# Performance work log

Measured on AMD Instinct MI355X. Metric: run time of the kernel, lower is better.

The kernel has to match this reference:

```python
import jax, jax.numpy as jnp
import numpy as np

NEG_INF = -1000000000.0

N, T, D, H = 2, 4096, 512, 8
S = D // H  # size_per_head = 64


def setup_inputs() -> dict:
    key = jax.random.key(0)
    ks = jax.random.split(key, 6)
    scale = 1.0 / np.sqrt(D)
    return {
        "query": jax.random.normal(ks[0], (N, T, D), dtype=jnp.float32),
        "reference": jax.random.normal(ks[1], (N, T, D), dtype=jnp.float32),
        "padding_mask": jnp.zeros((N, 1, 1, T), dtype=jnp.float32),
        "Wq": jax.random.normal(ks[2], (D, H, S), dtype=jnp.float32) * scale,
        "Wk": jax.random.normal(ks[3], (D, H, S), dtype=jnp.float32) * scale,
        "Wv": jax.random.normal(ks[4], (D, H, S), dtype=jnp.float32) * scale,
        "Wo": jax.random.normal(ks[5], (H, S, D), dtype=jnp.float32) * scale,
    }


def reference(query, reference, padding_mask, Wq, Wk, Wv, Wo):
    # split projections: [N,T,D] x [D,H,S] -> [N,T,H,S]
    q = jnp.einsum("NTD,DHS->NTHS", query, Wq) * (S ** -0.5)
    k = jnp.einsum("NTD,DHS->NTHS", reference, Wk)
    v = jnp.einsum("NTD,DHS->NTHS", reference, Wv)
    # scores [N,H,Q,R]; mask is 0/1, scaled by NEG_INF (as in source)
    scores = jnp.einsum("NQHS,NRHS->NHQR", q, k) + padding_mask * NEG_INF
    probs = jax.nn.softmax(scores, axis=3)
    # dropout is identity (training=False)
    ctx = jnp.einsum("NHQR,NRHS->NQHS", probs, v)
    # merge projection: [N,Q,H,S] x [H,S,D] -> [N,Q,D]
    return jnp.einsum("NTHS,HSD->NTD", ctx, Wo)
```

## Files before the change

### kernel.cpp

```cpp
#include <hip/hip_runtime.h>
#include <stdint.h>

using u16    = unsigned short;
using u32    = unsigned int;
using short8 = __attribute__((ext_vector_type(8))) short;
using s16x4  = __attribute__((ext_vector_type(4))) short;
using f32x4  = __attribute__((ext_vector_type(4))) float;
using f32x16 = __attribute__((ext_vector_type(16))) float;
using i32x4  = __attribute__((ext_vector_type(4))) int;

constexpr float LOG2E = 1.44269504088896340736f;


__device__ __forceinline__ u16 f2bf(float f) {
  uint32_t u = __builtin_bit_cast(uint32_t, f);
  return (u16)((u + 0x7fffu + ((u >> 16) & 1u)) >> 16);
}

__device__ __forceinline__ void gload16(const void* g, void* l) {
  __builtin_amdgcn_global_load_lds(
      (const __attribute__((address_space(1))) unsigned int*)g,
      (__attribute__((address_space(3))) unsigned int*)l, 16, 0, 0);
}

__device__ __forceinline__ u32 cvtpk_bf16(float lo, float hi) {
  u32 r;
  asm("v_cvt_pk_bf16_f32 %0, %1, %2" : "=v"(r) : "v"(lo), "v"(hi));
  return r;
}

__device__ __forceinline__ f32x16 zero16() {
  f32x16 z;
#pragma unroll
  for (int i = 0; i < 16; ++i) z[i] = 0.f;
  return z;
}

__device__ __forceinline__ short8 ldfrag(const u16* s, int row, int kbyte) {
  int phys = (row << 7) + (kbyte ^ ((row & 7) << 4));
  return *(const short8*)((const char*)s + phys);
}

__global__ __launch_bounds__(256) void prep_kernel(
    const float4* __restrict__ qin, const float4* __restrict__ rin,
    const float* __restrict__ mask,
    const float* __restrict__ wq, const float* __restrict__ wk,
    const float* __restrict__ wv, const float* __restrict__ wo,
    u16* __restrict__ xq, u16* __restrict__ xr,
    u16* __restrict__ wqt, u16* __restrict__ wkt,
    u16* __restrict__ wvt, u16* __restrict__ wot,
    u16* __restrict__ kfr, int* __restrict__ mflag) {
  const int gid = blockIdx.x * blockDim.x + threadIdx.x;
  const int stride = gridDim.x * blockDim.x;
  for (int i = gid; i < (2 * 4096 * 512) / 4; i += stride) {
    float4 a = qin[i], b = rin[i];
    s16x4 va = {(short)f2bf(a.x), (short)f2bf(a.y), (short)f2bf(a.z), (short)f2bf(a.w)};
    s16x4 vb = {(short)f2bf(b.x), (short)f2bf(b.y), (short)f2bf(b.z), (short)f2bf(b.w)};
    *(s16x4*)(xq + i * 4) = va;
    *(s16x4*)(xr + i * 4) = vb;
  }
  for (int i = gid; i < 512 * 512; i += stride) {
    int orow = i >> 9, ocol = i & 511;
    int si = ocol * 512 + orow;
    wqt[i] = f2bf(wq[si]);
    wkt[i] = f2bf(wk[si]);
    wvt[i] = f2bf(wv[si]);
    wot[i] = f2bf(wo[si]);
  }
  for (int i = gid; i < 16 * 4096; i += stride) {
    int head = i >> 12, key = i & 4095;
    int nn = head >> 3;
    float mv = mask[nn * 4096 + key];
    float mt = mv * (-1.0e9f * LOG2E);
    int tile = key >> 5, lqk = key & 31;
    u16* base = kfr + (((size_t)(head * 128 + tile)) * 5 + 4) * 512;
    u16* p0 = base + (size_t)lqk * 8;
    u16* p1 = base + (size_t)(32 + lqk) * 8;
    p0[0] = f2bf(mt);
#pragma unroll
    for (int j = 1; j < 8; ++j) p0[j] = 0;
#pragma unroll
    for (int j = 0; j < 8; ++j) p1[j] = 0;
    unsigned long long any = __ballot(mv != 0.0f);
    if ((threadIdx.x & 63) == 0 && any != 0ULL) atomicOr(mflag, 1);
  }
}

__device__ __forceinline__ void gemm_core(const u16* __restrict__ A, const u16* __restrict__ Bt,
                                          int K, u16* As, u16* Bs, int tm0, int tn0,
                                          f32x4 acc[4][4]) {
  const int tid = threadIdx.x;
  const int wv = tid >> 6, ln = tid & 63;
  const int lr = ln & 15, hi = ln >> 4;
  const int wr = wv >> 1, wc = wv & 1;
  const size_t rowbytes = (size_t)K * 2;
  for (int k0 = 0; k0 < K; k0 += 64) {
    __syncthreads();
    const char* Ab = (const char*)A + (size_t)tm0 * rowbytes + (size_t)k0 * 2;
    const char* Bb = (const char*)Bt + (size_t)tn0 * rowbytes + (size_t)k0 * 2;
#pragma unroll
    for (int c = 0; c < 4; ++c) {
      int lin = wv * 4096 + c * 1024 + ln * 16;
      int row = lin >> 7;
      int cb = (lin & 127) ^ ((row & 7) << 4);
      gload16(Ab + (size_t)row * rowbytes + cb, (char*)As + wv * 4096 + c * 1024);
      gload16(Bb + (size_t)row * rowbytes + cb, (char*)Bs + wv * 4096 + c * 1024);
    }
    __syncthreads();
#pragma unroll
    for (int ks = 0; ks < 2; ++ks) {
      short8 af[4], bf[4];
#pragma unroll
      for (int m = 0; m < 4; ++m) af[m] = ldfrag(As, wr * 64 + m * 16 + lr, ks * 64 + hi * 16);
#pragma unroll
      for (int n = 0; n < 4; ++n) bf[n] = ldfrag(Bs, wc * 64 + n * 16 + lr, ks * 64 + hi * 16);
#pragma unroll
      for (int m = 0; m < 4; ++m)
#pragma unroll
        for (int n = 0; n < 4; ++n)
          acc[m][n] = __builtin_amdgcn_mfma_f32_16x16x32_bf16(af[m], bf[n], acc[m][n], 0, 0, 0);
    }
  }
}

__global__ __launch_bounds__(256) void qkv_gemm(
    const u16* __restrict__ xq, const u16* __restrict__ xr,
    const u16* __restrict__ wqt, const u16* __restrict__ wkt, const u16* __restrict__ wvt,
    u16* __restrict__ qo, u16* __restrict__ kfr, u16* __restrict__ vfr) {
  __shared__ u16 As[128 * 64];
  __shared__ u16 Bs[128 * 64];
  const int z = blockIdx.z;
  const u16* A  = (z == 0) ? xq : xr;
  const u16* Bt = (z == 0) ? wqt : (z == 1) ? wkt : wvt;
  const int tm0 = blockIdx.x * 128, tn0 = blockIdx.y * 128;
  f32x4 acc[4][4];
#pragma unroll
  for (int m = 0; m < 4; ++m)
#pragma unroll
    for (int n = 0; n < 4; ++n) { f32x4 zz = {0.f, 0.f, 0.f, 0.f}; acc[m][n] = zz; }
  gemm_core(A, Bt, 512, As, Bs, tm0, tn0, acc);

  const int tid = threadIdx.x, wv = tid >> 6, ln = tid & 63, lr = ln & 15, hi = ln >> 4;
  const int wr = wv >> 1, wc = wv & 1;
  const float scale = (z == 0) ? 0.125f * LOG2E : 1.0f;
#pragma unroll
  for (int m = 0; m < 4; ++m) {
#pragma unroll
    for (int n = 0; n < 4; ++n) {
#pragma unroll
      for (int r = 0; r < 4; ++r) {
        int rg = tm0 + wr * 64 + m * 16 + hi * 4 + r;
        int cg = tn0 + wc * 64 + n * 16 + lr;
        int nb = rg >> 12, t = rg & 4095;
        int h = cg >> 6, s = cg & 63;
        int head = nb * 8 + h;
        u16 b = f2bf(acc[m][n][r] * scale);
        if (z == 0) {
          qo[((size_t)head * 4096 + t) * 64 + s] = b;
        } else if (z == 1) {
          int tile = t >> 5, lqk = t & 31;
          int ks = s >> 4, hh = (s >> 3) & 1, j = s & 7;
          kfr[((((size_t)(head * 128 + tile)) * 5 + ks) * 64 + hh * 32 + lqk) * 8 + j] = b;
        } else {
          int tile = t >> 5, key5 = t & 31;
          int c = key5 >> 4, w = key5 & 15;
          int hh2 = (w >> 2) & 1;
          int j2 = (w & 3) + ((w >> 3) << 2);
          int st = s >> 5, lqs = s & 31;
          vfr[((((size_t)(head * 128 + tile)) * 4 + c * 2 + st) * 64 + hh2 * 32 + lqs) * 8 + j2] = b;
        }
      }
    }
  }
}

__global__ __launch_bounds__(512, 2) void attn15_kernel(
    const u16* __restrict__ q, const char* __restrict__ kfr, const char* __restrict__ vfr,
    u16* __restrict__ ctx, const int* __restrict__ mflag) {
  __shared__ __align__(16) char smem[4 * 32 * 65 * 4];
  __shared__ float cl[4][64];
  float (*cmbraw)[32][64] = (float(*)[32][64])smem;
  float (*cmb2)[32][65]   = (float(*)[32][65])smem;
  const int id = blockIdx.x;
  const int xcd = id & 7, slot = id >> 3;
  const int head = xcd * 2 + (slot >> 4);
  const int qb = slot & 15;
  const int n = head >> 3, h = head & 7;
  const int tid = threadIdx.x, wv = tid >> 6, ln = tid & 63;
  const int lq = ln & 31, hi = ln >> 5, hi4 = hi * 4;
  const int qt = wv & 3, kg = wv >> 2;
  const int q0 = qb * 256 + qt * 64;
  const bool aug = (*mflag != 0);

  short8 qfa[5], qfb[5];
  {
    const char* qp = (const char*)(q + (size_t)head * 4096 * 64) + (size_t)(q0 + lq) * 128 + hi * 16;
#pragma unroll
    for (int ks = 0; ks < 4; ++ks) {
      qfa[ks] = *(const short8*)(qp + ks * 32);
      qfb[ks] = *(const short8*)(qp + 32 * 128 + ks * 32);
    }
    short8 z = {0, 0, 0, 0, 0, 0, 0, 0};
    if (hi == 0) z[0] = (short)0x3F80;
    qfa[4] = z;
    qfb[4] = z;
  }

  const char* kp = kfr + (size_t)head * 655360 + (size_t)(kg * 64) * 5120 + ln * 16;
  const char* vp = vfr + (size_t)head * 524288 + (size_t)(kg * 64) * 4096 + ln * 16;

  short8 kA[5];
#pragma unroll
  for (int s = 0; s < 4; ++s) kA[s] = *(const short8*)(kp + s * 1024);
  if (aug) kA[4] = *(const short8*)(kp + 4 * 1024);
  kp += 5120;

  f32x16 cacc0a = zero16(), cacc1a = zero16();
  f32x16 cacc0b = zero16(), cacc1b = zero16();
  f32x16 la = zero16(), lb = zero16();

  for (int it = 0; it < 64; ++it) {
    short8 vt[4];
#pragma unroll
    for (int s = 0; s < 4; ++s) vt[s] = *(const short8*)(vp + s * 1024);
    vp += 4096;

    f32x16 Sa = zero16(), Sb = zero16();
    __builtin_amdgcn_s_setprio(1);
#pragma unroll
    for (int ks = 0; ks < 4; ++ks) {
      Sa = __builtin_amdgcn_mfma_f32_32x32x16_bf16(kA[ks], qfa[ks], Sa, 0, 0, 0);
      Sb = __builtin_amdgcn_mfma_f32_32x32x16_bf16(kA[ks], qfb[ks], Sb, 0, 0, 0);
    }
    if (aug) {
      Sa = __builtin_amdgcn_mfma_f32_32x32x16_bf16(kA[4], qfa[4], Sa, 0, 0, 0);
      Sb = __builtin_amdgcn_mfma_f32_32x32x16_bf16(kA[4], qfb[4], Sb, 0, 0, 0);
    }
    __builtin_amdgcn_s_setprio(0);

    short8 kN[5];
#pragma unroll
    for (int s = 0; s < 4; ++s) kN[s] = *(const short8*)(kp + s * 1024);
    if (aug) kN[4] = *(const short8*)(kp + 4 * 1024);
    kp += 5120;

    float pa_[16], pb_[16];
#pragma unroll
    for (int r = 0; r < 16; ++r) { pa_[r] = __builtin_amdgcn_exp2f(Sa[r]); la[r] += pa_[r]; }
#pragma unroll
    for (int r = 0; r < 16; ++r) { pb_[r] = __builtin_amdgcn_exp2f(Sb[r]); lb[r] += pb_[r]; }

    short8 pA0, pA1, pB0, pB1;
    {
      i32x4 f0 = {(int)cvtpk_bf16(pa_[0], pa_[1]), (int)cvtpk_bf16(pa_[2], pa_[3]),
                  (int)cvtpk_bf16(pa_[4], pa_[5]), (int)cvtpk_bf16(pa_[6], pa_[7])};
      i32x4 f1 = {(int)cvtpk_bf16(pa_[8], pa_[9]), (int)cvtpk_bf16(pa_[10], pa_[11]),
                  (int)cvtpk_bf16(pa_[12], pa_[13]), (int)cvtpk_bf16(pa_[14], pa_[15])};
      i32x4 g0 = {(int)cvtpk_bf16(pb_[0], pb_[1]), (int)cvtpk_bf16(pb_[2], pb_[3]),
                  (int)cvtpk_bf16(pb_[4], pb_[5]), (int)cvtpk_bf16(pb_[6], pb_[7])};
      i32x4 g1 = {(int)cvtpk_bf16(pb_[8], pb_[9]), (int)cvtpk_bf16(pb_[10], pb_[11]),
                  (int)cvtpk_bf16(pb_[12], pb_[13]), (int)cvtpk_bf16(pb_[14], pb_[15])};
      pA0 = __builtin_bit_cast(short8, f0);
      pA1 = __builtin_bit_cast(short8, f1);
      pB0 = __builtin_bit_cast(short8, g0);
      pB1 = __builtin_bit_cast(short8, g1);
    }

    __builtin_amdgcn_s_setprio(1);
    cacc0a = __builtin_amdgcn_mfma_f32_32x32x16_bf16(vt[0], pA0, cacc0a, 0, 0, 0);
    cacc1a = __builtin_amdgcn_mfma_f32_32x32x16_bf16(vt[1], pA0, cacc1a, 0, 0, 0);
    cacc0b = __builtin_amdgcn_mfma_f32_32x32x16_bf16(vt[0], pB0, cacc0b, 0, 0, 0);
    cacc1b = __builtin_amdgcn_mfma_f32_32x32x16_bf16(vt[1], pB0, cacc1b, 0, 0, 0);
    cacc0a = __builtin_amdgcn_mfma_f32_32x32x16_bf16(vt[2], pA1, cacc0a, 0, 0, 0);
    cacc1a = __builtin_amdgcn_mfma_f32_32x32x16_bf16(vt[3], pA1, cacc1a, 0, 0, 0);
    cacc0b = __builtin_amdgcn_mfma_f32_32x32x16_bf16(vt[2], pB1, cacc0b, 0, 0, 0);
    cacc1b = __builtin_amdgcn_mfma_f32_32x32x16_bf16(vt[3], pB1, cacc1b, 0, 0, 0);
    __builtin_amdgcn_s_setprio(0);

#pragma unroll
    for (int s = 0; s < 4; ++s) kA[s] = kN[s];
    if (aug) kA[4] = kN[4];
  }

  float lra, lrb;
  {
    float ta[16], tb[16];
#pragma unroll
    for (int r = 0; r < 16; ++r) { ta[r] = la[r]; tb[r] = lb[r]; }
#pragma unroll
    for (int d = 8; d > 0; d >>= 1)
#pragma unroll
      for (int r = 0; r < d; ++r) { ta[r] += ta[r + d]; tb[r] += tb[r + d]; }
    lra = ta[0] + __shfl_xor(ta[0], 32);
    lrb = tb[0] + __shfl_xor(tb[0], 32);
  }

  auto epilogue = [&](f32x16& c0, f32x16& c1, float lr, int qofs) {
    if (kg == 1) {
#pragma unroll
      for (int r = 0; r < 16; ++r) {
        cmbraw[qt][r][ln] = c0[r];
        cmbraw[qt][r + 16][ln] = c1[r];
      }
      cl[qt][ln] = lr;
    }
    __syncthreads();
    if (kg == 0) {
#pragma unroll
      for (int r = 0; r < 16; ++r) {
        c0[r] += cmbraw[qt][r][ln];
        c1[r] += cmbraw[qt][r + 16][ln];
      }
      lr += cl[qt][ln];
    }
    __syncthreads();
    if (kg == 0) {
      float li = 1.0f / lr;
#pragma unroll
      for (int r = 0; r < 16; ++r) {
        int s0 = (r & 3) + ((r >> 2) << 3) + hi4;
        cmb2[qt][lq][s0] = c0[r] * li;
        cmb2[qt][lq][32 + s0] = c1[r] * li;
      }
    }
    __syncthreads();
    {
      u16* cpx = ctx + (size_t)(n * 4096 + qb * 256 + qt * 64 + qofs) * 512 + h * 64;
#pragma unroll
      for (int rr = 0; rr < 16; ++rr) {
        int qq = kg * 16 + rr;
        cpx[(size_t)qq * 512 + ln] = f2bf(cmb2[qt][qq][ln]);
      }
    }
    __syncthreads();
  };
  epilogue(cacc0a, cacc1a, lra, 0);
  epilogue(cacc0b, cacc1b, lrb, 32);
}

__global__ __launch_bounds__(256) void out_gemm(
    const u16* __restrict__ ctx, const u16* __restrict__ wot, float* __restrict__ out) {
  __shared__ u16 As[128 * 64];
  __shared__ u16 Bs[128 * 64];
  const int tm0 = blockIdx.x * 128, tn0 = blockIdx.y * 128;
  f32x4 acc[4][4];
#pragma unroll
  for (int m = 0; m < 4; ++m)
#pragma unroll
    for (int n = 0; n < 4; ++n) { f32x4 zz = {0.f, 0.f, 0.f, 0.f}; acc[m][n] = zz; }
  gemm_core(ctx, wot, 512, As, Bs, tm0, tn0, acc);

  const int tid = threadIdx.x, wv = tid >> 6, ln = tid & 63, lr = ln & 15, hi = ln >> 4;
  const int wr = wv >> 1, wc = wv & 1;
#pragma unroll
  for (int m = 0; m < 4; ++m)
#pragma unroll
    for (int n = 0; n < 4; ++n)
#pragma unroll
      for (int r = 0; r < 4; ++r) {
        int rg = tm0 + wr * 64 + m * 16 + hi * 4 + r;
        int cg = tn0 + wc * 64 + n * 16 + lr;
        out[(size_t)rg * 512 + cg] = acc[m][n][r];
      }
}

extern "C" void kernel_launch(void* const* d_in, const int* in_sizes, int n_in,
                              void* d_out, int out_size, void* d_ws, size_t ws_size,
                              hipStream_t stream) {
  (void)in_sizes; (void)n_in; (void)out_size; (void)ws_size;
  const float* qin  = (const float*)d_in[0];
  const float* rin  = (const float*)d_in[1];
  const float* mask = (const float*)d_in[2];
  const float* wq   = (const float*)d_in[3];
  const float* wk   = (const float*)d_in[4];
  const float* wv   = (const float*)d_in[5];
  const float* wo   = (const float*)d_in[6];

  char* ws = (char*)d_ws;
  u16* xq   = (u16*)(ws + 0);
  u16* ctx  = (u16*)(ws + 0);
  u16* xr   = (u16*)(ws + 8388608);
  u16* wqt  = (u16*)(ws + 16777216);
  u16* wkt  = (u16*)(ws + 17301504);
  u16* wvt  = (u16*)(ws + 17825792);
  u16* wot  = (u16*)(ws + 18350080);
  u16* qo   = (u16*)(ws + 18874368);
  u16* kfr  = (u16*)(ws + 27262976);
  u16* vfr  = (u16*)(ws + 37748736);
  int* mflag = (int*)(ws + 46137344);

  hipMemsetAsync(mflag, 0, 4, stream);
  prep_kernel<<<2048, 256, 0, stream>>>((const float4*)qin, (const float4*)rin, mask,
                                        wq, wk, wv, wo, xq, xr, wqt, wkt, wvt, wot,
                                        kfr, mflag);
  qkv_gemm<<<dim3(64, 4, 3), 256, 0, stream>>>(xq, xr, wqt, wkt, wvt, qo, kfr, vfr);
  attn15_kernel<<<256, 512, 0, stream>>>(qo, (const char*)kfr, (const char*)vfr, ctx, mflag);
  out_gemm<<<dim3(64, 4), 256, 0, stream>>>(ctx, wot, (float*)d_out);
}
```

Baseline: 127.6 us.

## Coalesce weight transpose via LDS, split softmax halves, retile output GEMM

The weight transpose in the prep kernel now stages 64x64 tiles through shared memory, so both its global reads and writes are coalesced instead of strided. The attention loop processes the two query halves one after the other (QK, exp, PV for A, then for B), which can interleave exp work with MFMA and lower register pressure. The output GEMM moves to 128x64 tiles with its own inline loop, doubling the grid to 512 blocks for better CU occupancy at the cost of more A-tile reloads.

```diff
diff --git a/kernel.cpp b/kernel.cpp
--- a/kernel.cpp
+++ b/kernel.cpp
@@ -50,6 +50,7 @@
     u16* __restrict__ wqt, u16* __restrict__ wkt,
     u16* __restrict__ wvt, u16* __restrict__ wot,
     u16* __restrict__ kfr, int* __restrict__ mflag) {
+  __shared__ float tlds[64][65];
   const int gid = blockIdx.x * blockDim.x + threadIdx.x;
   const int stride = gridDim.x * blockDim.x;
   for (int i = gid; i < (2 * 4096 * 512) / 4; i += stride) {
@@ -59,13 +60,23 @@
     *(s16x4*)(xq + i * 4) = va;
     *(s16x4*)(xr + i * 4) = vb;
   }
-  for (int i = gid; i < 512 * 512; i += stride) {
-    int orow = i >> 9, ocol = i & 511;
-    int si = ocol * 512 + orow;
-    wqt[i] = f2bf(wq[si]);
-    wkt[i] = f2bf(wk[si]);
-    wvt[i] = f2bf(wv[si]);
-    wot[i] = f2bf(wo[si]);
+  if (blockIdx.x < 256) {
+    const int tid = threadIdx.x;
+    const int w = blockIdx.x >> 6, tpos = blockIdx.x & 63;
+    const int tr = tpos >> 3, tc = tpos & 7;
+    const float* src = (w == 0) ? wq : (w == 1) ? wk : (w == 2) ? wv : wo;
+    u16* dst = (w == 0) ? wqt : (w == 1) ? wkt : (w == 2) ? wvt : wot;
+#pragma unroll
+    for (int p = 0; p < 16; ++p) {
+      int r = p * 4 + (tid >> 6), c = tid & 63;
+      tlds[r][c] = src[(size_t)(tr * 64 + r) * 512 + tc * 64 + c];
+    }
+    __syncthreads();
+#pragma unroll
+    for (int p = 0; p < 16; ++p) {
+      int c2 = p * 4 + (tid >> 6), r2 = tid & 63;
+      dst[(size_t)(tc * 64 + c2) * 512 + tr * 64 + r2] = f2bf(tlds[r2][c2]);
+    }
   }
   for (int i = gid; i < 16 * 4096; i += stride) {
     int head = i >> 12, key = i & 4095;
@@ -174,7 +185,7 @@
   }
 }
 
-__global__ __launch_bounds__(512, 2) void attn15_kernel(
+__global__ __launch_bounds__(512, 2) void attn16_kernel(
     const u16* __restrict__ q, const char* __restrict__ kfr, const char* __restrict__ vfr,
     u16* __restrict__ ctx, const int* __restrict__ mflag) {
   __shared__ __align__(16) char smem[4 * 32 * 65 * 4];
@@ -228,14 +239,13 @@
     f32x16 Sa = zero16(), Sb = zero16();
     __builtin_amdgcn_s_setprio(1);
 #pragma unroll
-    for (int ks = 0; ks < 4; ++ks) {
+    for (int ks = 0; ks < 4; ++ks)
       Sa = __builtin_amdgcn_mfma_f32_32x32x16_bf16(kA[ks], qfa[ks], Sa, 0, 0, 0);
+    if (aug) Sa = __builtin_amdgcn_mfma_f32_32x32x16_bf16(kA[4], qfa[4], Sa, 0, 0, 0);
+#pragma unroll
+    for (int ks = 0; ks < 4; ++ks)
       Sb = __builtin_amdgcn_mfma_f32_32x32x16_bf16(kA[ks], qfb[ks], Sb, 0, 0, 0);
-    }
-    if (aug) {
-      Sa = __builtin_amdgcn_mfma_f32_32x32x16_bf16(kA[4], qfa[4], Sa, 0, 0, 0);
-      Sb = __builtin_amdgcn_mfma_f32_32x32x16_bf16(kA[4], qfb[4], Sb, 0, 0, 0);
-    }
+    if (aug) Sb = __builtin_amdgcn_mfma_f32_32x32x16_bf16(kA[4], qfb[4], Sb, 0, 0, 0);
     __builtin_amdgcn_s_setprio(0);
 
     short8 kN[5];
@@ -244,35 +254,42 @@
     if (aug) kN[4] = *(const short8*)(kp + 4 * 1024);
     kp += 5120;
 
-    float pa_[16], pb_[16];
+    float pa_[16];
 #pragma unroll
     for (int r = 0; r < 16; ++r) { pa_[r] = __builtin_amdgcn_exp2f(Sa[r]); la[r] += pa_[r]; }
-#pragma unroll
-    for (int r = 0; r < 16; ++r) { pb_[r] = __builtin_amdgcn_exp2f(Sb[r]); lb[r] += pb_[r]; }
-
-    short8 pA0, pA1, pB0, pB1;
+    short8 pA0, pA1;
     {
       i32x4 f0 = {(int)cvtpk_bf16(pa_[0], pa_[1]), (int)cvtpk_bf16(pa_[2], pa_[3]),
                   (int)cvtpk_bf16(pa_[4], pa_[5]), (int)cvtpk_bf16(pa_[6], pa_[7])};
       i32x4 f1 = {(int)cvtpk_bf16(pa_[8], pa_[9]), (int)cvtpk_bf16(pa_[10], pa_[11]),
                   (int)cvtpk_bf16(pa_[12], pa_[13]), (int)cvtpk_bf16(pa_[14], pa_[15])};
+      pA0 = __builtin_bit_cast(short8, f0);
+      pA1 = __builtin_bit_cast(short8, f1);
+    }
+
+    __builtin_amdgcn_s_setprio(1);
+    cacc0a = __builtin_amdgcn_mfma_f32_32x32x16_bf16(vt[0], pA0, cacc0a, 0, 0, 0);
+    cacc1a = __builtin_amdgcn_mfma_f32_32x32x16_bf16(vt[1], pA0, cacc1a, 0, 0, 0);
+    cacc0a = __builtin_amdgcn_mfma_f32_32x32x16_bf16(vt[2], pA1, cacc0a, 0, 0, 0);
+    cacc1a = __builtin_amdgcn_mfma_f32_32x32x16_bf16(vt[3], pA1, cacc1a, 0, 0, 0);
+    __builtin_amdgcn_s_setprio(0);
+
+    float pb_[16];
+#pragma unroll
+    for (int r = 0; r < 16; ++r) { pb_[r] = __builtin_amdgcn_exp2f(Sb[r]); lb[r] += pb_[r]; }
+    short8 pB0, pB1;
+    {
       i32x4 g0 = {(int)cvtpk_bf16(pb_[0], pb_[1]), (int)cvtpk_bf16(pb_[2], pb_[3]),
                   (int)cvtpk_bf16(pb_[4], pb_[5]), (int)cvtpk_bf16(pb_[6], pb_[7])};
       i32x4 g1 = {(int)cvtpk_bf16(pb_[8], pb_[9]), (int)cvtpk_bf16(pb_[10], pb_[11]),
                   (int)cvtpk_bf16(pb_[12], pb_[13]), (int)cvtpk_bf16(pb_[14], pb_[15])};
-      pA0 = __builtin_bit_cast(short8, f0);
-      pA1 = __builtin_bit_cast(short8, f1);
       pB0 = __builtin_bit_cast(short8, g0);
       pB1 = __builtin_bit_cast(short8, g1);
     }
 
     __builtin_amdgcn_s_setprio(1);
-    cacc0a = __builtin_amdgcn_mfma_f32_32x32x16_bf16(vt[0], pA0, cacc0a, 0, 0, 0);
-    cacc1a = __builtin_amdgcn_mfma_f32_32x32x16_bf16(vt[1], pA0, cacc1a, 0, 0, 0);
     cacc0b = __builtin_amdgcn_mfma_f32_32x32x16_bf16(vt[0], pB0, cacc0b, 0, 0, 0);
     cacc1b = __builtin_amdgcn_mfma_f32_32x32x16_bf16(vt[1], pB0, cacc1b, 0, 0, 0);
-    cacc0a = __builtin_amdgcn_mfma_f32_32x32x16_bf16(vt[2], pA1, cacc0a, 0, 0, 0);
-    cacc1a = __builtin_amdgcn_mfma_f32_32x32x16_bf16(vt[3], pA1, cacc1a, 0, 0, 0);
     cacc0b = __builtin_amdgcn_mfma_f32_32x32x16_bf16(vt[2], pB1, cacc0b, 0, 0, 0);
     cacc1b = __builtin_amdgcn_mfma_f32_32x32x16_bf16(vt[3], pB1, cacc1b, 0, 0, 0);
     __builtin_amdgcn_s_setprio(0);
@@ -341,25 +358,58 @@
 __global__ __launch_bounds__(256) void out_gemm(
     const u16* __restrict__ ctx, const u16* __restrict__ wot, float* __restrict__ out) {
   __shared__ u16 As[128 * 64];
-  __shared__ u16 Bs[128 * 64];
-  const int tm0 = blockIdx.x * 128, tn0 = blockIdx.y * 128;
-  f32x4 acc[4][4];
-#pragma unroll
-  for (int m = 0; m < 4; ++m)
+  __shared__ u16 Bs[64 * 64];
+  const int tm0 = blockIdx.x * 128, tn0 = blockIdx.y * 64;
+  const int tid = threadIdx.x, wv = tid >> 6, ln = tid & 63;
+  const int lr = ln & 15, hi = ln >> 4;
+  f32x4 acc[2][4];
+#pragma unroll
+  for (int m = 0; m < 2; ++m)
 #pragma unroll
     for (int n = 0; n < 4; ++n) { f32x4 zz = {0.f, 0.f, 0.f, 0.f}; acc[m][n] = zz; }
-  gemm_core(ctx, wot, 512, As, Bs, tm0, tn0, acc);
-
-  const int tid = threadIdx.x, wv = tid >> 6, ln = tid & 63, lr = ln & 15, hi = ln >> 4;
-  const int wr = wv >> 1, wc = wv & 1;
-#pragma unroll
-  for (int m = 0; m < 4; ++m)
+
+  const size_t rowbytes = 1024;
+  for (int k0 = 0; k0 < 512; k0 += 64) {
+    __syncthreads();
+    const char* Ab = (const char*)ctx + (size_t)tm0 * rowbytes + (size_t)k0 * 2;
+    const char* Bb = (const char*)wot + (size_t)tn0 * rowbytes + (size_t)k0 * 2;
+#pragma unroll
+    for (int c = 0; c < 4; ++c) {
+      int lin = wv * 4096 + c * 1024 + ln * 16;
+      int row = lin >> 7;
+      int cb = (lin & 127) ^ ((row & 7) << 4);
+      gload16(Ab + (size_t)row * rowbytes + cb, (char*)As + wv * 4096 + c * 1024);
+    }
+#pragma unroll
+    for (int c = 0; c < 2; ++c) {
+      int lin = wv * 2048 + c * 1024 + ln * 16;
+      int row = lin >> 7;
+      int cb = (lin & 127) ^ ((row & 7) << 4);
+      gload16(Bb + (size_t)row * rowbytes + cb, (char*)Bs + wv * 2048 + c * 1024);
+    }
+    __syncthreads();
+#pragma unroll
+    for (int ks = 0; ks < 2; ++ks) {
+      short8 af[2], bf[4];
+#pragma unroll
+      for (int m = 0; m < 2; ++m) af[m] = ldfrag(As, wv * 32 + m * 16 + lr, ks * 64 + hi * 16);
+#pragma unroll
+      for (int n = 0; n < 4; ++n) bf[n] = ldfrag(Bs, n * 16 + lr, ks * 64 + hi * 16);
+#pragma unroll
+      for (int m = 0; m < 2; ++m)
+#pragma unroll
+        for (int n = 0; n < 4; ++n)
+          acc[m][n] = __builtin_amdgcn_mfma_f32_16x16x32_bf16(af[m], bf[n], acc[m][n], 0, 0, 0);
+    }
+  }
+#pragma unroll
+  for (int m = 0; m < 2; ++m)
 #pragma unroll
     for (int n = 0; n < 4; ++n)
 #pragma unroll
       for (int r = 0; r < 4; ++r) {
-        int rg = tm0 + wr * 64 + m * 16 + hi * 4 + r;
-        int cg = tn0 + wc * 64 + n * 16 + lr;
+        int rg = tm0 + wv * 32 + m * 16 + hi * 4 + r;
+        int cg = tn0 + n * 16 + lr;
         out[(size_t)rg * 512 + cg] = acc[m][n][r];
       }
 }
@@ -394,6 +444,6 @@
                                         wq, wk, wv, wo, xq, xr, wqt, wkt, wvt, wot,
                                         kfr, mflag);
   qkv_gemm<<<dim3(64, 4, 3), 256, 0, stream>>>(xq, xr, wqt, wkt, wvt, qo, kfr, vfr);
-  attn15_kernel<<<256, 512, 0, stream>>>(qo, (const char*)kfr, (const char*)vfr, ctx, mflag);
-  out_gemm<<<dim3(64, 4), 256, 0, stream>>>(ctx, wot, (float*)d_out);
-}
+  attn16_kernel<<<256, 512, 0, stream>>>(qo, (const char*)kfr, (const char*)vfr, ctx, mflag);
+  out_gemm<<<dim3(64, 8), 256, 0, stream>>>(ctx, wot, (float*)d_out);
+}
```

After: 122.2 us. 4.2% less time.
